# Kernel tuning notes

Hardware: AMD Instinct MI355X
Metric: run time of the kernel (lower is better)

The kernel has to match this reference:

```python
import jax, jax.numpy as jnp
import numpy as np

B, S, I, H, O = 32, 64, 256, 256, 128


def setup_inputs() -> dict:
    key = jax.random.key(0)
    ks = jax.random.split(key, 8)
    init_k = 1.0 / np.sqrt(H)
    F = H + I
    return {
        "sentence": jax.random.normal(ks[0], (B, S, I), dtype=jnp.float32),
        "weight": jax.random.uniform(ks[1], (H, F), minval=-init_k, maxval=init_k, dtype=jnp.float32),
        "weight_lambda": jax.random.uniform(ks[2], (H, F), minval=0.0, maxval=1.0, dtype=jnp.float32),
        "weight_gamma": jax.random.uniform(ks[3], (H, F), minval=-0.001 * init_k, maxval=0.001 * init_k, dtype=jnp.float32),
        "bias": jax.random.uniform(ks[4], (H,), minval=-init_k, maxval=init_k, dtype=jnp.float32),
        "out_w": jax.random.uniform(ks[5], (O, H), minval=-init_k, maxval=init_k, dtype=jnp.float32),
        "out_b": jax.random.uniform(ks[6], (O,), minval=-init_k, maxval=init_k, dtype=jnp.float32),
    }


def reference(sentence, weight, weight_lambda, weight_gamma, bias, out_w, out_b):
    b, s, i = sentence.shape
    h_dim = weight.shape[0]
    f_dim = weight.shape[1]  # h_dim + i
    h0 = jnp.zeros((b, h_dim), dtype=sentence.dtype)
    f0 = jnp.zeros((b, h_dim, f_dim), dtype=sentence.dtype)

    def step(carry, x_t):
        h, f = carry
        total_input = jnp.concatenate([x_t, h], axis=1)          # (b, f_dim)
        total_weights = weight + f                                # (b, h, f_dim)
        pre = jnp.einsum('bf,bhf->bh', total_input, total_weights)
        norm = jnp.sqrt(jnp.sum(total_weights * total_weights, axis=2)) + 1e-16  # (b, h)
        h_new = jnp.tanh(pre / norm + bias)
        f_new = weight_lambda * (f / norm[..., None]) + \
                weight_gamma * jnp.einsum('bh,bf->bhf', h_new, total_input)
        return (h_new, f_new), None

    (h_fin, f_fin), _ = jax.lax.scan(step, (h0, f0), jnp.swapaxes(sentence, 0, 1))
    tag_space = h_fin @ out_w.T + out_b
    return tag_space, h_fin, f_fin
```

## Files before the change

kernel.cpp:

```cpp
#include <hip/hip_runtime.h>

#define Bq 32
#define Sq 64
#define Iq 256
#define Hq 256
#define Oq 128
#define Fq 512
#define WPB 8
#define NT 512
#define PRE_S 56

__global__ __launch_bounds__(NT, 2) void stpn_main(
    const float* __restrict__ x,
    const float* __restrict__ w,
    const float* __restrict__ wl,
    const float* __restrict__ wgm,
    const float* __restrict__ bias,
    const float* __restrict__ ow,
    const float* __restrict__ ob,
    float* __restrict__ out,
    unsigned long long* __restrict__ hb)
{
    const int blk   = blockIdx.x;
    const int b     = blk & 31;
    const int chunk = blk >> 5;
    const int h0    = chunk * 32;
    const int tid   = threadIdx.x;
    const int lr    = tid & 15;
    const int r     = tid >> 4;
    const int row   = h0 + r;

    __shared__ float ti[2][Fq];
    __shared__ float xall[PRE_S * Iq];

    float fw[32], fl[32], fg[32], ff[32];
    const size_t rowoff = (size_t)row * Fq;
#pragma unroll
    for (int j = 0; j < 8; ++j) {
        const int c = 4 * lr + 64 * j;
        *(float4*)&fw[4*j] = *(const float4*)(w   + rowoff + c);
        *(float4*)&fl[4*j] = *(const float4*)(wl  + rowoff + c);
        *(float4*)&fg[4*j] = *(const float4*)(wgm + rowoff + c);
    }
#pragma unroll
    for (int j = 0; j < 32; ++j) ff[j] = 0.f;

    {
        const float4* xs = (const float4*)(x + (size_t)b * Sq * Iq);
        float4* xd = (float4*)xall;
#pragma unroll
        for (int k = 0; k < (PRE_S * Iq / 4) / NT; ++k)
            xd[tid + NT * k] = xs[tid + NT * k];
    }
    const float brow = bias[row];
    const float* xb = x + (size_t)b * Sq * Iq;

    for (int t = 0; t < Sq; ++t) {
        const int p = t & 1;
        if (tid < Iq) {
            if (t >= PRE_S) ti[p][tid] = xb[(size_t)t * Iq + tid];
        } else {
            const int hh = tid - Iq;
            float hv = 0.f;
            if (t > 0) {
                unsigned long long* slot =
                    hb + (size_t)((t - 1) & 1) * Bq * Hq + (size_t)b * Hq + hh;
                unsigned long long v;
                do {
                    v = __hip_atomic_load(slot, __ATOMIC_RELAXED,
                                          __HIP_MEMORY_SCOPE_AGENT);
                } while ((unsigned)(v >> 32) != (unsigned)t);
                hv = __uint_as_float((unsigned)(v & 0xffffffffu));
            }
            ti[p][Iq + hh] = hv;
        }
        __syncthreads();

        const float* xpart = (t < PRE_S) ? (xall + t * Iq) : &ti[p][0];
        const float* hpart = &ti[p][Iq];

        float pre = 0.f, nsq = 0.f;
#pragma unroll
        for (int j = 0; j < 4; ++j) {
            const float4 tv = *(const float4*)&xpart[4 * lr + 64 * j];
            float tw;
            tw = fw[4*j+0] + ff[4*j+0]; pre = fmaf(tv.x, tw, pre); nsq = fmaf(tw, tw, nsq);
            tw = fw[4*j+1] + ff[4*j+1]; pre = fmaf(tv.y, tw, pre); nsq = fmaf(tw, tw, nsq);
            tw = fw[4*j+2] + ff[4*j+2]; pre = fmaf(tv.z, tw, pre); nsq = fmaf(tw, tw, nsq);
            tw = fw[4*j+3] + ff[4*j+3]; pre = fmaf(tv.w, tw, pre); nsq = fmaf(tw, tw, nsq);
        }
#pragma unroll
        for (int j = 4; j < 8; ++j) {
            const float4 tv = *(const float4*)&hpart[4 * lr + 64 * (j - 4)];
            float tw;
            tw = fw[4*j+0] + ff[4*j+0]; pre = fmaf(tv.x, tw, pre); nsq = fmaf(tw, tw, nsq);
            tw = fw[4*j+1] + ff[4*j+1]; pre = fmaf(tv.y, tw, pre); nsq = fmaf(tw, tw, nsq);
            tw = fw[4*j+2] + ff[4*j+2]; pre = fmaf(tv.z, tw, pre); nsq = fmaf(tw, tw, nsq);
            tw = fw[4*j+3] + ff[4*j+3]; pre = fmaf(tv.w, tw, pre); nsq = fmaf(tw, tw, nsq);
        }
#pragma unroll
        for (int m = 1; m < 16; m <<= 1) {
            pre += __shfl_xor(pre, m, 16);
            nsq += __shfl_xor(nsq, m, 16);
        }
        const float inv = __fdividef(1.0f, sqrtf(nsq) + 1e-16f);
        const float hn  = tanhf(fmaf(pre, inv, brow));

        if (lr == 0) {
            const unsigned long long pk =
                ((unsigned long long)(unsigned)(t + 1) << 32) |
                (unsigned long long)__float_as_uint(hn);
            __hip_atomic_store(
                hb + (size_t)p * Bq * Hq + (size_t)b * Hq + row, pk,
                __ATOMIC_RELAXED, __HIP_MEMORY_SCOPE_AGENT);
        }

#pragma unroll
        for (int j = 0; j < 4; ++j) {
            const float4 tv = *(const float4*)&xpart[4 * lr + 64 * j];
            ff[4*j+0] = fmaf(fl[4*j+0], ff[4*j+0] * inv, fg[4*j+0] * (hn * tv.x));
            ff[4*j+1] = fmaf(fl[4*j+1], ff[4*j+1] * inv, fg[4*j+1] * (hn * tv.y));
            ff[4*j+2] = fmaf(fl[4*j+2], ff[4*j+2] * inv, fg[4*j+2] * (hn * tv.z));
            ff[4*j+3] = fmaf(fl[4*j+3], ff[4*j+3] * inv, fg[4*j+3] * (hn * tv.w));
        }
#pragma unroll
        for (int j = 4; j < 8; ++j) {
            const float4 tv = *(const float4*)&hpart[4 * lr + 64 * (j - 4)];
            ff[4*j+0] = fmaf(fl[4*j+0], ff[4*j+0] * inv, fg[4*j+0] * (hn * tv.x));
            ff[4*j+1] = fmaf(fl[4*j+1], ff[4*j+1] * inv, fg[4*j+1] * (hn * tv.y));
            ff[4*j+2] = fmaf(fl[4*j+2], ff[4*j+2] * inv, fg[4*j+2] * (hn * tv.z));
            ff[4*j+3] = fmaf(fl[4*j+3], ff[4*j+3] * inv, fg[4*j+3] * (hn * tv.w));
        }
    }

    float* fo = out + Bq * Oq + Bq * Hq + (size_t)b * Hq * Fq + rowoff;
#pragma unroll
    for (int j = 0; j < 8; ++j) {
        const int c = 4 * lr + 64 * j;
        *(float4*)(fo + c) = *(const float4*)&ff[4*j];
    }

    if (chunk == 0) {
        if (tid < Hq) {
            unsigned long long* slot =
                hb + (size_t)1 * Bq * Hq + (size_t)b * Hq + tid;
            unsigned long long v;
            do {
                v = __hip_atomic_load(slot, __ATOMIC_RELAXED,
                                      __HIP_MEMORY_SCOPE_AGENT);
            } while ((unsigned)(v >> 32) != (unsigned)Sq);
            const float hv = __uint_as_float((unsigned)(v & 0xffffffffu));
            ti[0][tid] = hv;
            out[Bq * Oq + (size_t)b * Hq + tid] = hv;
        }
        __syncthreads();
        const int o = tid >> 2;
        const int l = tid & 3;
        const float* wr = ow + (size_t)o * Hq;
        float acc = 0.f;
#pragma unroll
        for (int k = 0; k < 16; ++k) {
            const int cc = 16 * k + 4 * l;
            const float4 w4 = *(const float4*)(wr + cc);
            const float4 h4 = *(const float4*)&ti[0][cc];
            acc += w4.x * h4.x + w4.y * h4.y + w4.z * h4.z + w4.w * h4.w;
        }
        acc += __shfl_xor(acc, 1, 4);
        acc += __shfl_xor(acc, 2, 4);
        if (l == 0) out[(size_t)b * Oq + o] = acc + ob[o];
    }
}

extern "C" void kernel_launch(void* const* d_in, const int* in_sizes, int n_in,
                              void* d_out, int out_size, void* d_ws, size_t ws_size,
                              hipStream_t stream)
{
    const float* x    = (const float*)d_in[0];
    const float* w    = (const float*)d_in[1];
    const float* wl   = (const float*)d_in[2];
    const float* wgm  = (const float*)d_in[3];
    const float* bias = (const float*)d_in[4];
    const float* ow   = (const float*)d_in[5];
    const float* ob   = (const float*)d_in[6];
    float* out = (float*)d_out;

    hipMemsetAsync(d_ws, 0, 2 * Bq * Hq * sizeof(unsigned long long), stream);

    stpn_main<<<Bq * WPB, NT, 0, stream>>>(x, w, wl, wgm, bias, ow, ob, out,
                                           (unsigned long long*)d_ws);
}
```

Measured before the change: 154.3 us.

## Split h polling across idle threads, bypass global for own rows, fast tanh

Each block now writes its own 32 hidden outputs straight into the next step's shared buffer instead of reading them back through global memory. Polling for the remaining hidden values is shared between the x-loading threads (idle while x is preloaded) and the h threads, which coordinate through a shared-memory flag array. It also swaps tanhf for an exp-based fast tanh and the sqrt+divide for a reciprocal sqrt, which drops the 1e-16 epsilon and changes precision slightly. The cooperative polling relies on a volatile shared flag with racy writes and adds s_sleep calls, which could add latency.

After: 174.2 us. 12.8% more time.

```diff
diff --git a/kernel.cpp b/kernel.cpp
--- a/kernel.cpp
+++ b/kernel.cpp
@@ -9,6 +9,11 @@
 #define WPB 8
 #define NT 512
 #define PRE_S 56
+
+__device__ __forceinline__ float fast_tanh(float v) {
+    const float e = __expf(2.0f * v);
+    return 1.0f - __fdividef(2.0f, e + 1.0f);
+}
 
 __global__ __launch_bounds__(NT, 2) void stpn_main(
     const float* __restrict__ x,
@@ -32,6 +37,7 @@
 
     __shared__ float ti[2][Fq];
     __shared__ float xall[PRE_S * Iq];
+    __shared__ int   pollflag[Hq];
 
     float fw[32], fl[32], fg[32], ff[32];
     const size_t rowoff = (size_t)row * Fq;
@@ -52,27 +58,55 @@
         for (int k = 0; k < (PRE_S * Iq / 4) / NT; ++k)
             xd[tid + NT * k] = xs[tid + NT * k];
     }
+    if (tid < Hq) pollflag[tid] = 0;
     const float brow = bias[row];
     const float* xb = x + (size_t)b * Sq * Iq;
 
     for (int t = 0; t < Sq; ++t) {
         const int p = t & 1;
         if (tid < Iq) {
-            if (t >= PRE_S) ti[p][tid] = xb[(size_t)t * Iq + tid];
+            if (t >= PRE_S) {
+                ti[p][tid] = xb[(size_t)t * Iq + tid];
+            } else if (t > 0 && tid < Hq - 32) {
+                const int hh = tid + (tid >= h0 ? 32 : 0);
+                unsigned long long* slot =
+                    hb + (size_t)((t - 1) & 1) * Bq * Hq + (size_t)b * Hq + hh;
+                volatile int* fl_ = &pollflag[hh];
+                __builtin_amdgcn_s_sleep(5);
+                if (*fl_ != t) {
+                    do {
+                        unsigned long long v =
+                            __hip_atomic_load(slot, __ATOMIC_RELAXED,
+                                              __HIP_MEMORY_SCOPE_AGENT);
+                        if ((unsigned)(v >> 32) == (unsigned)t) {
+                            ti[p][Iq + hh] =
+                                __uint_as_float((unsigned)(v & 0xffffffffu));
+                            *fl_ = t;
+                            break;
+                        }
+                    } while (*fl_ != t);
+                }
+            }
         } else {
             const int hh = tid - Iq;
-            float hv = 0.f;
-            if (t > 0) {
+            if (t == 0) {
+                ti[p][Iq + hh] = 0.f;
+            } else if (hh < h0 || hh >= h0 + 32) {
                 unsigned long long* slot =
                     hb + (size_t)((t - 1) & 1) * Bq * Hq + (size_t)b * Hq + hh;
-                unsigned long long v;
+                volatile int* fl_ = &pollflag[hh];
                 do {
-                    v = __hip_atomic_load(slot, __ATOMIC_RELAXED,
+                    unsigned long long v =
+                        __hip_atomic_load(slot, __ATOMIC_RELAXED,
                                           __HIP_MEMORY_SCOPE_AGENT);
-                } while ((unsigned)(v >> 32) != (unsigned)t);
-                hv = __uint_as_float((unsigned)(v & 0xffffffffu));
+                    if ((unsigned)(v >> 32) == (unsigned)t) {
+                        ti[p][Iq + hh] =
+                            __uint_as_float((unsigned)(v & 0xffffffffu));
+                        *fl_ = t;
+                        break;
+                    }
+                } while (*fl_ != t);
             }
-            ti[p][Iq + hh] = hv;
         }
         __syncthreads();
 
@@ -103,10 +137,12 @@
             pre += __shfl_xor(pre, m, 16);
             nsq += __shfl_xor(nsq, m, 16);
         }
-        const float inv = __fdividef(1.0f, sqrtf(nsq) + 1e-16f);
-        const float hn  = tanhf(fmaf(pre, inv, brow));
+        const float inv = __frsqrt_rn(nsq);
+        const float hn  = fast_tanh(fmaf(pre, inv, brow));
 
         if (lr == 0) {
+            if (t < Sq - 1)
+                ti[(t + 1) & 1][Iq + row] = hn;
             const unsigned long long pk =
                 ((unsigned long long)(unsigned)(t + 1) << 32) |
                 (unsigned long long)__float_as_uint(hn);
```

## Add L2-cached fast-path hidden-state exchange, local self-write, and fast tanh/rsqrt

Applied to the files above, without the earlier changes.

Hidden-state exchange between blocks now polls a second buffer with inline-asm loads and stores marked sc0, aimed at a cheaper L2 path, and falls back to the agent-scope atomic copy. Each block writes its own 32 hidden values straight into shared memory, so it no longer polls for rows it produced itself. tanh is replaced by an exp-based formula and the norm reciprocal by rsqrt, which drops the 1e-16 epsilon. The goal is to cut per-timestep cross-block sync latency, at the cost of duplicate stores, a larger memset, and dependence on ISA cache-coherence semantics.

Result: slower. 172.9 us (+12.1%).

```diff
diff --git a/kernel.cpp b/kernel.cpp
--- a/kernel.cpp
+++ b/kernel.cpp
@@ -9,6 +9,25 @@
 #define WPB 8
 #define NT 512
 #define PRE_S 56
+
+__device__ __forceinline__ float fast_tanh(float v) {
+    const float e = __expf(2.0f * v);
+    return 1.0f - __fdividef(2.0f, e + 1.0f);
+}
+
+__device__ __forceinline__ unsigned long long load_u64_l2(
+    const unsigned long long* p) {
+    unsigned long long v;
+    asm volatile("global_load_dwordx2 %0, %1, off sc0\n\t"
+                 "s_waitcnt vmcnt(0)"
+                 : "=v"(v) : "v"(p) : "memory");
+    return v;
+}
+__device__ __forceinline__ void store_u64_l2(unsigned long long* p,
+                                             unsigned long long v) {
+    asm volatile("global_store_dwordx2 %0, %1, off" :: "v"(p), "v"(v)
+                 : "memory");
+}
 
 __global__ __launch_bounds__(NT, 2) void stpn_main(
     const float* __restrict__ x,
@@ -30,6 +49,9 @@
     const int r     = tid >> 4;
     const int row   = h0 + r;
 
+    unsigned long long* hsafe = hb;
+    unsigned long long* hfast = hb + 2 * Bq * Hq;
+
     __shared__ float ti[2][Fq];
     __shared__ float xall[PRE_S * Iq];
 
@@ -61,18 +83,23 @@
             if (t >= PRE_S) ti[p][tid] = xb[(size_t)t * Iq + tid];
         } else {
             const int hh = tid - Iq;
-            float hv = 0.f;
-            if (t > 0) {
-                unsigned long long* slot =
-                    hb + (size_t)((t - 1) & 1) * Bq * Hq + (size_t)b * Hq + hh;
+            if (t == 0) {
+                ti[p][Iq + hh] = 0.f;
+            } else if (hh < h0 || hh >= h0 + 32) {
+                const size_t idx =
+                    (size_t)((t - 1) & 1) * Bq * Hq + (size_t)b * Hq + hh;
+                const unsigned long long* fs = hfast + idx;
+                const unsigned long long* ss = hsafe + idx;
                 unsigned long long v;
-                do {
-                    v = __hip_atomic_load(slot, __ATOMIC_RELAXED,
+                for (;;) {
+                    v = load_u64_l2(fs);
+                    if ((unsigned)(v >> 32) == (unsigned)t) break;
+                    v = __hip_atomic_load(ss, __ATOMIC_RELAXED,
                                           __HIP_MEMORY_SCOPE_AGENT);
-                } while ((unsigned)(v >> 32) != (unsigned)t);
-                hv = __uint_as_float((unsigned)(v & 0xffffffffu));
+                    if ((unsigned)(v >> 32) == (unsigned)t) break;
+                }
+                ti[p][Iq + hh] = __uint_as_float((unsigned)(v & 0xffffffffu));
             }
-            ti[p][Iq + hh] = hv;
         }
         __syncthreads();
 
@@ -103,16 +130,19 @@
             pre += __shfl_xor(pre, m, 16);
             nsq += __shfl_xor(nsq, m, 16);
         }
-        const float inv = __fdividef(1.0f, sqrtf(nsq) + 1e-16f);
-        const float hn  = tanhf(fmaf(pre, inv, brow));
+        const float inv = __frsqrt_rn(nsq);
+        const float hn  = fast_tanh(fmaf(pre, inv, brow));
 
         if (lr == 0) {
+            if (t < Sq - 1)
+                ti[(t + 1) & 1][Iq + row] = hn;
             const unsigned long long pk =
                 ((unsigned long long)(unsigned)(t + 1) << 32) |
                 (unsigned long long)__float_as_uint(hn);
-            __hip_atomic_store(
-                hb + (size_t)p * Bq * Hq + (size_t)b * Hq + row, pk,
-                __ATOMIC_RELAXED, __HIP_MEMORY_SCOPE_AGENT);
+            const size_t idx = (size_t)p * Bq * Hq + (size_t)b * Hq + row;
+            store_u64_l2(hfast + idx, pk);
+            __hip_atomic_store(hsafe + idx, pk, __ATOMIC_RELAXED,
+                               __HIP_MEMORY_SCOPE_AGENT);
         }
 
 #pragma unroll
@@ -142,13 +172,17 @@
 
     if (chunk == 0) {
         if (tid < Hq) {
-            unsigned long long* slot =
-                hb + (size_t)1 * Bq * Hq + (size_t)b * Hq + tid;
+            const size_t idx = (size_t)1 * Bq * Hq + (size_t)b * Hq + tid;
+            const unsigned long long* fs = hfast + idx;
+            const unsigned long long* ss = hsafe + idx;
             unsigned long long v;
-            do {
-                v = __hip_atomic_load(slot, __ATOMIC_RELAXED,
+            for (;;) {
+                v = load_u64_l2(fs);
+                if ((unsigned)(v >> 32) == (unsigned)Sq) break;
+                v = __hip_atomic_load(ss, __ATOMIC_RELAXED,
                                       __HIP_MEMORY_SCOPE_AGENT);
-            } while ((unsigned)(v >> 32) != (unsigned)Sq);
+                if ((unsigned)(v >> 32) == (unsigned)Sq) break;
+            }
             const float hv = __uint_as_float((unsigned)(v & 0xffffffffu));
             ti[0][tid] = hv;
             out[Bq * Oq + (size_t)b * Hq + tid] = hv;
@@ -184,7 +218,7 @@
     const float* ob   = (const float*)d_in[6];
     float* out = (float*)d_out;
 
-    hipMemsetAsync(d_ws, 0, 2 * Bq * Hq * sizeof(unsigned long long), stream);
+    hipMemsetAsync(d_ws, 0, 4 * Bq * Hq * sizeof(unsigned long long), stream);
 
     stpn_main<<<Bq * WPB, NT, 0, stream>>>(x, w, wl, wgm, bias, ow, ob, out,
                                            (unsigned long long*)d_ws);
```

## Drop shared x prefetch and move next-step input load after the f update

Applied to the files above, without the earlier changes.

Removes the large 56-step shared-memory preload of x, which shrinks LDS use per block. The next step's x slice and the spin-wait on h are moved to the end of each iteration, after the f update, with a single barrier per step. The intent is to overlap the f update with other blocks producing h and to cut LDS pressure. In exchange, every step now reads x from global memory and the spin-wait stays on the critical path.

New measurement: 193.7 us. +25.5%, slower.

```diff
diff --git a/kernel.cpp b/kernel.cpp
--- a/kernel.cpp
+++ b/kernel.cpp
@@ -8,7 +8,6 @@
 #define Fq 512
 #define WPB 8
 #define NT 512
-#define PRE_S 56
 
 __global__ __launch_bounds__(NT, 2) void stpn_main(
     const float* __restrict__ x,
@@ -31,7 +30,6 @@
     const int row   = h0 + r;
 
     __shared__ float ti[2][Fq];
-    __shared__ float xall[PRE_S * Iq];
 
     float fw[32], fl[32], fg[32], ff[32];
     const size_t rowoff = (size_t)row * Fq;
@@ -45,38 +43,16 @@
 #pragma unroll
     for (int j = 0; j < 32; ++j) ff[j] = 0.f;
 
-    {
-        const float4* xs = (const float4*)(x + (size_t)b * Sq * Iq);
-        float4* xd = (float4*)xall;
-#pragma unroll
-        for (int k = 0; k < (PRE_S * Iq / 4) / NT; ++k)
-            xd[tid + NT * k] = xs[tid + NT * k];
-    }
     const float brow = bias[row];
     const float* xb = x + (size_t)b * Sq * Iq;
 
+    if (tid < Iq) ti[0][tid] = xb[tid];
+    else          ti[0][tid] = 0.f;
+    __syncthreads();
+
     for (int t = 0; t < Sq; ++t) {
         const int p = t & 1;
-        if (tid < Iq) {
-            if (t >= PRE_S) ti[p][tid] = xb[(size_t)t * Iq + tid];
-        } else {
-            const int hh = tid - Iq;
-            float hv = 0.f;
-            if (t > 0) {
-                unsigned long long* slot =
-                    hb + (size_t)((t - 1) & 1) * Bq * Hq + (size_t)b * Hq + hh;
-                unsigned long long v;
-                do {
-                    v = __hip_atomic_load(slot, __ATOMIC_RELAXED,
-                                          __HIP_MEMORY_SCOPE_AGENT);
-                } while ((unsigned)(v >> 32) != (unsigned)t);
-                hv = __uint_as_float((unsigned)(v & 0xffffffffu));
-            }
-            ti[p][Iq + hh] = hv;
-        }
-        __syncthreads();
-
-        const float* xpart = (t < PRE_S) ? (xall + t * Iq) : &ti[p][0];
+        const float* xpart = &ti[p][0];
         const float* hpart = &ti[p][Iq];
 
         float pre = 0.f, nsq = 0.f;
@@ -131,6 +107,23 @@
             ff[4*j+2] = fmaf(fl[4*j+2], ff[4*j+2] * inv, fg[4*j+2] * (hn * tv.z));
             ff[4*j+3] = fmaf(fl[4*j+3], ff[4*j+3] * inv, fg[4*j+3] * (hn * tv.w));
         }
+
+        if (t < Sq - 1) {
+            if (tid < Iq) {
+                ti[p ^ 1][tid] = xb[(size_t)(t + 1) * Iq + tid];
+            } else {
+                const int hh = tid - Iq;
+                const unsigned long long* slot =
+                    hb + (size_t)p * Bq * Hq + (size_t)b * Hq + hh;
+                unsigned long long v;
+                do {
+                    v = __hip_atomic_load(slot, __ATOMIC_RELAXED,
+                                          __HIP_MEMORY_SCOPE_AGENT);
+                } while ((unsigned)(v >> 32) != (unsigned)(t + 1));
+                ti[p ^ 1][Iq + hh] = __uint_as_float((unsigned)(v & 0xffffffffu));
+            }
+        }
+        __syncthreads();
     }
 
     float* fo = out + Bq * Oq + Bq * Hq + (size_t)b * Hq * Fq + rowoff;
@@ -142,7 +135,7 @@
 
     if (chunk == 0) {
         if (tid < Hq) {
-            unsigned long long* slot =
+            const unsigned long long* slot =
                 hb + (size_t)1 * Bq * Hq + (size_t)b * Hq + tid;
             unsigned long long v;
             do {
```
